# Optimization experiments

Measured on AMD Instinct MI355X. Metric: run time of the kernel, lower is better.

The kernel has to match this reference:

```python
import jax, jax.numpy as jnp
import numpy as np
import math


def _proj(x, W, b):
    # 1x1 conv: x [B,C,H,W], W [O,C], b [O]
    return jnp.einsum('bchw,oc->bohw', x, W) + b[None, :, None, None]


def _head(x, Win, bin_, Wh, bh, Wout, bout):
    # in-layer ProjConv (no skip) with ReLU
    h = jax.nn.relu(_proj(x, Win, bin_))
    # hidden ProjConv layers with skip connection (kernel_size == 1 branch)
    for i in range(Wh.shape[0]):  # static small layer count
        h = h + jax.nn.relu(_proj(h, Wh[i], bh[i]))
    # out-layer ProjConv (logits, no activation)
    return _proj(h, Wout, bout)


def _forward(x, cls_Win, cls_bin, cls_Wh, cls_bh, cls_Wout, cls_bout,
             obj_Win, obj_bin, obj_Wh, obj_bh, obj_Wout, obj_bout,
             box_Win, box_bin, box_Wh, box_bh, box_Wout, box_bout,
             pos_Win, pos_bin, pos_Wh, pos_bh, pos_Wout, pos_bout,
             ins_Win, ins_bin, ins_Wh, ins_bh, ins_Wout, ins_bout):
    cls_logits = _head(x, cls_Win, cls_bin, cls_Wh, cls_bh, cls_Wout, cls_bout)  # [B,81,H,W]
    obj_logits = _head(x, obj_Win, obj_bin, obj_Wh, obj_bh, obj_Wout, obj_bout)  # [B,2,H,W]
    box_logits = _head(x, box_Win, box_bin, box_Wh, box_bh, box_Wout, box_bout)  # [B,4,H,W]
    pos_feats = _head(x, pos_Win, pos_bin, pos_Wh, pos_bh, pos_Wout, pos_bout)   # [B,64,H,W]
    ins_feats = _head(x, ins_Win, ins_bin, ins_Wh, ins_bh, ins_Wout, ins_bout)   # [B,128,H,W]
    return jnp.concatenate([cls_logits, obj_logits, box_logits, pos_feats, ins_feats], axis=1)


def setup_inputs() -> dict:
    key = jax.random.key(0)
    ks = iter(jax.random.split(key, 64))
    F, Cin, L = 64, 64, 2
    d = {'x': jax.random.normal(next(ks), (4, Cin, 256, 256), dtype=jnp.float32)}
    outs = {'cls': 81, 'obj': 2, 'box': 4, 'pos': 64, 'ins': 128}
    prior_bias = -math.log((1.0 - 0.01) / 0.01)  # prior_prob init for cls/obj out biases
    bias0 = {'cls': prior_bias, 'obj': prior_bias, 'box': 0.0, 'pos': 0.0, 'ins': 0.0}
    for name, od in outs.items():
        d[name + '_Win'] = (jax.random.normal(next(ks), (F, Cin)) * 0.05).astype(jnp.float32)
        d[name + '_bin'] = jnp.zeros((F,), dtype=jnp.float32)
        d[name + '_Wh'] = (jax.random.normal(next(ks), (L, F, F)) * 0.05).astype(jnp.float32)
        d[name + '_bh'] = jnp.zeros((L, F), dtype=jnp.float32)
        d[name + '_Wout'] = (jax.random.normal(next(ks), (od, F)) * 0.05).astype(jnp.float32)
        d[name + '_bout'] = jnp.full((od,), bias0[name], dtype=jnp.float32)
    return d


def reference(x, cls_Win, cls_bin, cls_Wh, cls_bh, cls_Wout, cls_bout,
              obj_Win, obj_bin, obj_Wh, obj_bh, obj_Wout, obj_bout,
              box_Win, box_bin, box_Wh, box_bh, box_Wout, box_bout,
              pos_Win, pos_bin, pos_Wh, pos_bh, pos_Wout, pos_bout,
              ins_Win, ins_bin, ins_Wh, ins_bh, ins_Wout, ins_bout):
    return _forward(x, cls_Win, cls_bin, cls_Wh, cls_bh, cls_Wout, cls_bout,
                    obj_Win, obj_bin, obj_Wh, obj_bh, obj_Wout, obj_bout,
                    box_Win, box_bin, box_Wh, box_bh, box_Wout, box_bout,
                    pos_Win, pos_bin, pos_Wh, pos_bh, pos_Wout, pos_bout,
                    ins_Win, ins_bin, ins_Wh, ins_bh, ins_Wout, ins_bout)
```

## Files before the change

kernel.cpp:

```cpp
#include <hip/hip_runtime.h>

typedef unsigned short u16;
typedef unsigned int   u32;
typedef __attribute__((ext_vector_type(8)))  short bf16x8;
typedef __attribute__((ext_vector_type(4)))  float f32x4;
typedef __attribute__((ext_vector_type(16))) float f32x16;

constexpr int NPIX = 4 * 65536;

__device__ constexpr int OD_[5]   = {81, 2, 4, 64, 128};
__device__ constexpr int NFO_[5]  = {3, 1, 1, 2, 4};
__device__ constexpr int COFF_[5] = {0, 81, 83, 87, 151};
__device__ constexpr int FB_[5]   = {0, 36, 64, 92, 124};

struct PW { const float* w[20]; };
struct PB { const float* x; float* out; const u16* wf; const float* b[20]; };

__device__ __forceinline__ void split2(float v, short& hi, short& lo) {
    u32 bi = __builtin_bit_cast(u32, v);
    float lof = v - __builtin_bit_cast(float, bi & 0xffff0000u);
    hi = (short)(bi >> 16);
    lo = (short)(__builtin_bit_cast(u32, lof) >> 16);
}

__global__ __launch_bounds__(256) void prep_weights(PW wp, u16* wf) {
    int slot = blockIdx.x * 256 + threadIdx.x;
    if (slot >= 164 * 64) return;
    int frag = slot >> 6, lane = slot & 63;
    int fb = 0, seg = 0;
    for (int s = 0; s < 20; ++s) {
        int h = s >> 2, ly = s & 3;
        int cnt = (ly < 3) ? 8 : 4 * NFO_[h];
        if (frag < fb + cnt) { seg = s; break; }
        fb += cnt;
    }
    int h = seg >> 2, ly = seg & 3;
    int lf = frag - fb;
    int nf = lf >> 2, ks = lf & 3;
    int col  = nf * 32 + (lane & 31);
    int ksrc = ks * 16 + (lane >> 5) * 8;
    int rows = (ly < 3) ? 64 : OD_[h];
    const float* W = wp.w[seg];
    float wv[8];
    if (col < rows) {
        const float4* q = reinterpret_cast<const float4*>(W + col * 64 + ksrc);
        float4 a = q[0], c = q[1];
        wv[0]=a.x; wv[1]=a.y; wv[2]=a.z; wv[3]=a.w;
        wv[4]=c.x; wv[5]=c.y; wv[6]=c.z; wv[7]=c.w;
    } else {
#pragma unroll
        for (int j = 0; j < 8; ++j) wv[j] = 0.f;
    }
    bf16x8 vh, vl;
#pragma unroll
    for (int j = 0; j < 8; ++j) { short a, b; split2(wv[j], a, b); vh[j]=a; vl[j]=b; }
    u16* dst = wf + (size_t)frag * 1024 + lane * 8;
    *(bf16x8*)dst         = vh;
    *(bf16x8*)(dst + 512) = vl;
}

__device__ __forceinline__ u32 hswz(int row, int ch) {
    return (u32)((row << 8) + (ch << 2)) ^ (u32)((row & 7) << 4);
}

__device__ __forceinline__ void load_a(const char* H, int arow, int ks, int hb,
                                       bf16x8& ah, bf16x8& al) {
    u32 o0 = hswz(arow, ks * 16 + hb);
    f32x4 q0 = *(const f32x4*)(H + o0);
    f32x4 q1 = *(const f32x4*)(H + (o0 ^ 16));
    float qa[8] = {q0.x, q0.y, q0.z, q0.w, q1.x, q1.y, q1.z, q1.w};
#pragma unroll
    for (int j = 0; j < 8; ++j) { short a, b; split2(qa[j], a, b); ah[j]=a; al[j]=b; }
}

template<bool SKIP, bool FROM_LDS>
__device__ __forceinline__ void proj_layer(const bf16x8* Xh, const bf16x8* Xl,
                                           char* H, const u16* wfb,
                                           const float* bias, int l) {
    int hb = (l >> 5) * 8, arow = l & 31, hi4 = (l >> 5) * 4;
    f32x16 acc0, acc1;
#pragma unroll
    for (int i = 0; i < 16; ++i) { acc0[i] = 0.f; acc1[i] = 0.f; }
#pragma unroll
    for (int ks = 0; ks < 4; ++ks) {
        bf16x8 ah, al;
        if (FROM_LDS) load_a(H, arow, ks, hb, ah, al);
        else          { ah = Xh[ks]; al = Xl[ks]; }
        const u16* f0 = wfb + (size_t)ks * 1024;
        const u16* f1 = wfb + (size_t)(4 + ks) * 1024;
        bf16x8 b0h = *(const bf16x8*)f0, b0l = *(const bf16x8*)(f0 + 512);
        bf16x8 b1h = *(const bf16x8*)f1, b1l = *(const bf16x8*)(f1 + 512);
        acc0 = __builtin_amdgcn_mfma_f32_32x32x16_bf16(ah, b0h, acc0, 0, 0, 0);
        acc0 = __builtin_amdgcn_mfma_f32_32x32x16_bf16(ah, b0l, acc0, 0, 0, 0);
        acc0 = __builtin_amdgcn_mfma_f32_32x32x16_bf16(al, b0h, acc0, 0, 0, 0);
        acc1 = __builtin_amdgcn_mfma_f32_32x32x16_bf16(ah, b1h, acc1, 0, 0, 0);
        acc1 = __builtin_amdgcn_mfma_f32_32x32x16_bf16(ah, b1l, acc1, 0, 0, 0);
        acc1 = __builtin_amdgcn_mfma_f32_32x32x16_bf16(al, b1h, acc1, 0, 0, 0);
    }
    auto epi = [&](const f32x16& acc, int nf) {
        int ch = nf * 32 + (l & 31);
        float bv = bias[ch];
#pragma unroll
        for (int reg = 0; reg < 16; ++reg) {
            int row = (reg & 3) + 8 * (reg >> 2) + hi4;
            u32 off = hswz(row, ch);
            float v = fmaxf(acc[reg] + bv, 0.f);
            if (SKIP) v += *(const float*)(H + off);
            *(float*)(H + off) = v;
        }
    };
    epi(acc0, 0);
    epi(acc1, 1);
}

__device__ __forceinline__ void out_layer(const char* H, const u16* wfb,
                                          const float* bout, int od, int nfo,
                                          float* op_base, int l) {
    int hb = (l >> 5) * 8, arow = l & 31, hi4 = (l >> 5) * 4;
    bf16x8 Ah[4], Al[4];
#pragma unroll
    for (int ks = 0; ks < 4; ++ks) load_a(H, arow, ks, hb, Ah[ks], Al[ks]);
    for (int nf = 0; nf < nfo; ++nf) {
        f32x16 acc;
#pragma unroll
        for (int i = 0; i < 16; ++i) acc[i] = 0.f;
#pragma unroll
        for (int ks = 0; ks < 4; ++ks) {
            const u16* f = wfb + (size_t)(nf * 4 + ks) * 1024;
            bf16x8 bh = *(const bf16x8*)f, bl = *(const bf16x8*)(f + 512);
            acc = __builtin_amdgcn_mfma_f32_32x32x16_bf16(Ah[ks], bh, acc, 0, 0, 0);
            acc = __builtin_amdgcn_mfma_f32_32x32x16_bf16(Ah[ks], bl, acc, 0, 0, 0);
            acc = __builtin_amdgcn_mfma_f32_32x32x16_bf16(Al[ks], bh, acc, 0, 0, 0);
        }
        int col = nf * 32 + (l & 31);
        if (col < od) {
            float bv = bout[col];
            float* op = op_base + ((size_t)col << 16);
#pragma unroll
            for (int g = 0; g < 4; ++g) {
                int r0 = 8 * g + hi4;
                f32x4 st = {acc[4*g+0] + bv, acc[4*g+1] + bv,
                            acc[4*g+2] + bv, acc[4*g+3] + bv};
                __builtin_nontemporal_store(st, (f32x4*)(op + r0));
            }
        }
    }
}

__global__ __launch_bounds__(256, 4) void heads_main(PB p) {
    __shared__ char Hs[4][8192];
    int tid = threadIdx.x, w = tid >> 6, l = tid & 63;
    char* H = Hs[w];
    int p0 = blockIdx.x * 128 + w * 32;
    int b = p0 >> 16, hw0 = p0 & 65535;
    int hb = (l >> 5) * 8;
    const float* xb = p.x + ((size_t)(b * 64) << 16) + hw0 + (l & 31);

    bf16x8 Xh[4], Xl[4];
#pragma unroll
    for (int ks = 0; ks < 4; ++ks)
#pragma unroll
        for (int j = 0; j < 8; ++j) {
            int ch = ks * 16 + hb + j;
            float v = xb[(size_t)ch << 16];
            short a, c; split2(v, a, c);
            Xh[ks][j] = a; Xl[ks][j] = c;
        }

    const u16* wfl = p.wf + l * 8;
    for (int h = 0; h < 5; ++h) {
        const u16* wfb = wfl + (size_t)FB_[h] * 1024;
        proj_layer<false, false>(Xh, Xl, H, wfb,              p.b[4*h+0], l);
        proj_layer<true,  true >(Xh, Xl, H, wfb +  8 * 1024,  p.b[4*h+1], l);
        proj_layer<true,  true >(Xh, Xl, H, wfb + 16 * 1024,  p.b[4*h+2], l);
        float* op = p.out + ((size_t)(b * 279 + COFF_[h]) << 16) + hw0;
        out_layer(H, wfb + 24 * 1024, p.b[4*h+3], OD_[h], NFO_[h], op, l);
    }
}

extern "C" void kernel_launch(void* const* d_in, const int* in_sizes, int n_in,
                              void* d_out, int out_size, void* d_ws, size_t ws_size,
                              hipStream_t stream)
{
    auto A = [&](int i) { return (const float*)d_in[i]; };
    PW wp; PB pb;
    for (int h = 0; h < 5; ++h) {
        wp.w[4*h+0] = A(1 + 6*h + 0);
        wp.w[4*h+1] = A(1 + 6*h + 2);
        wp.w[4*h+2] = A(1 + 6*h + 2) + 4096;
        wp.w[4*h+3] = A(1 + 6*h + 4);
        pb.b[4*h+0] = A(1 + 6*h + 1);
        pb.b[4*h+1] = A(1 + 6*h + 3);
        pb.b[4*h+2] = A(1 + 6*h + 3) + 64;
        pb.b[4*h+3] = A(1 + 6*h + 5);
    }
    u16* wf = (u16*)d_ws;
    pb.x = (const float*)d_in[0];
    pb.out = (float*)d_out;
    pb.wf = wf;

    prep_weights<<<41, 256, 0, stream>>>(wp, wf);
    heads_main<<<NPIX / 128, 256, 0, stream>>>(pb);
}
```

Baseline: 609.7 us.

## Software-pipeline weight fragment loads across layers with templated per-head bodies

Restructures each head into a fully unrolled templated body that keeps an 8-deep register ring of weight fragments, prefetching the next fragment right after each MFMA triple so global weight loads overlap compute across layer boundaries. The head loop is unrolled with compile-time output fragment counts. It also replaces nontemporal output stores with normal stores and lowers the occupancy hint from 4 to 3 waves per SIMD to make room for the extra registers, which may reduce latency hiding from other waves.

```diff
diff --git a/kernel.cpp b/kernel.cpp
--- a/kernel.cpp
+++ b/kernel.cpp
@@ -10,7 +10,6 @@
 
 __device__ constexpr int OD_[5]   = {81, 2, 4, 64, 128};
 __device__ constexpr int NFO_[5]  = {3, 1, 1, 2, 4};
-__device__ constexpr int COFF_[5] = {0, 81, 83, 87, 151};
 __device__ constexpr int FB_[5]   = {0, 36, 64, 92, 124};
 
 struct PW { const float* w[20]; };
@@ -73,64 +72,90 @@
     for (int j = 0; j < 8; ++j) { short a, b; split2(qa[j], a, b); ah[j]=a; al[j]=b; }
 }
 
-template<bool SKIP, bool FROM_LDS>
-__device__ __forceinline__ void proj_layer(const bf16x8* Xh, const bf16x8* Xl,
-                                           char* H, const u16* wfb,
-                                           const float* bias, int l) {
+#define MFMA3(ACC, AH, AL, BH, BL)                                              \
+    ACC = __builtin_amdgcn_mfma_f32_32x32x16_bf16(AH, BH, ACC, 0, 0, 0);        \
+    ACC = __builtin_amdgcn_mfma_f32_32x32x16_bf16(AH, BL, ACC, 0, 0, 0);        \
+    ACC = __builtin_amdgcn_mfma_f32_32x32x16_bf16(AL, BH, ACC, 0, 0, 0);
+
+template<int NFO>
+__device__ __forceinline__ void head_body(const bf16x8* Xh, const bf16x8* Xl,
+                                          char* H, const u16* wfb,
+                                          const float* b0, const float* b1,
+                                          const float* b2, const float* bout,
+                                          int od, float* op_base, int l) {
+    constexpr int NFRAG = 24 + 4 * NFO;
     int hb = (l >> 5) * 8, arow = l & 31, hi4 = (l >> 5) * 4;
-    f32x16 acc0, acc1;
-#pragma unroll
-    for (int i = 0; i < 16; ++i) { acc0[i] = 0.f; acc1[i] = 0.f; }
-#pragma unroll
-    for (int ks = 0; ks < 4; ++ks) {
-        bf16x8 ah, al;
-        if (FROM_LDS) load_a(H, arow, ks, hb, ah, al);
-        else          { ah = Xh[ks]; al = Xl[ks]; }
-        const u16* f0 = wfb + (size_t)ks * 1024;
-        const u16* f1 = wfb + (size_t)(4 + ks) * 1024;
-        bf16x8 b0h = *(const bf16x8*)f0, b0l = *(const bf16x8*)(f0 + 512);
-        bf16x8 b1h = *(const bf16x8*)f1, b1l = *(const bf16x8*)(f1 + 512);
-        acc0 = __builtin_amdgcn_mfma_f32_32x32x16_bf16(ah, b0h, acc0, 0, 0, 0);
-        acc0 = __builtin_amdgcn_mfma_f32_32x32x16_bf16(ah, b0l, acc0, 0, 0, 0);
-        acc0 = __builtin_amdgcn_mfma_f32_32x32x16_bf16(al, b0h, acc0, 0, 0, 0);
-        acc1 = __builtin_amdgcn_mfma_f32_32x32x16_bf16(ah, b1h, acc1, 0, 0, 0);
-        acc1 = __builtin_amdgcn_mfma_f32_32x32x16_bf16(ah, b1l, acc1, 0, 0, 0);
-        acc1 = __builtin_amdgcn_mfma_f32_32x32x16_bf16(al, b1h, acc1, 0, 0, 0);
-    }
-    auto epi = [&](const f32x16& acc, int nf) {
-        int ch = nf * 32 + (l & 31);
-        float bv = bias[ch];
-#pragma unroll
-        for (int reg = 0; reg < 16; ++reg) {
-            int row = (reg & 3) + 8 * (reg >> 2) + hi4;
-            u32 off = hswz(row, ch);
-            float v = fmaxf(acc[reg] + bv, 0.f);
-            if (SKIP) v += *(const float*)(H + off);
-            *(float*)(H + off) = v;
-        }
-    };
-    epi(acc0, 0);
-    epi(acc1, 1);
-}
-
-__device__ __forceinline__ void out_layer(const char* H, const u16* wfb,
-                                          const float* bout, int od, int nfo,
-                                          float* op_base, int l) {
-    int hb = (l >> 5) * 8, arow = l & 31, hi4 = (l >> 5) * 4;
+
+    bf16x8 Ph[8], Pl[8];
+#pragma unroll
+    for (int f = 0; f < 8; ++f) {
+        const u16* fp = wfb + (size_t)f * 1024;
+        Ph[f] = *(const bf16x8*)fp;
+        Pl[f] = *(const bf16x8*)(fp + 512);
+    }
+
+#pragma unroll
+    for (int ly = 0; ly < 3; ++ly) {
+        bf16x8 Ah[4], Al[4];
+#pragma unroll
+        for (int ks = 0; ks < 4; ++ks) {
+            if (ly == 0) { Ah[ks] = Xh[ks]; Al[ks] = Xl[ks]; }
+            else         load_a(H, arow, ks, hb, Ah[ks], Al[ks]);
+        }
+        const float* bias = (ly == 0) ? b0 : ((ly == 1) ? b1 : b2);
+        f32x16 acc0, acc1;
+#pragma unroll
+        for (int i = 0; i < 16; ++i) { acc0[i] = 0.f; acc1[i] = 0.f; }
+#pragma unroll
+        for (int nf = 0; nf < 2; ++nf)
+#pragma unroll
+            for (int ks = 0; ks < 4; ++ks) {
+                int fi = ly * 8 + nf * 4 + ks;
+                int c  = fi & 7;
+                if (nf == 0) { MFMA3(acc0, Ah[ks], Al[ks], Ph[c], Pl[c]); }
+                else         { MFMA3(acc1, Ah[ks], Al[ks], Ph[c], Pl[c]); }
+                int nx = fi + 8;
+                if (nx < NFRAG) {
+                    const u16* fp = wfb + (size_t)nx * 1024;
+                    Ph[c] = *(const bf16x8*)fp;
+                    Pl[c] = *(const bf16x8*)(fp + 512);
+                }
+            }
+#pragma unroll
+        for (int nf = 0; nf < 2; ++nf) {
+            int ch = nf * 32 + (l & 31);
+            float bv = bias[ch];
+#pragma unroll
+            for (int reg = 0; reg < 16; ++reg) {
+                int row = (reg & 3) + 8 * (reg >> 2) + hi4;
+                u32 off = hswz(row, ch);
+                float a = (nf == 0) ? acc0[reg] : acc1[reg];
+                float v = fmaxf(a + bv, 0.f);
+                if (ly > 0) v += *(const float*)(H + off);
+                *(float*)(H + off) = v;
+            }
+        }
+    }
+
     bf16x8 Ah[4], Al[4];
 #pragma unroll
     for (int ks = 0; ks < 4; ++ks) load_a(H, arow, ks, hb, Ah[ks], Al[ks]);
-    for (int nf = 0; nf < nfo; ++nf) {
+#pragma unroll
+    for (int nf = 0; nf < NFO; ++nf) {
         f32x16 acc;
 #pragma unroll
         for (int i = 0; i < 16; ++i) acc[i] = 0.f;
 #pragma unroll
         for (int ks = 0; ks < 4; ++ks) {
-            const u16* f = wfb + (size_t)(nf * 4 + ks) * 1024;
-            bf16x8 bh = *(const bf16x8*)f, bl = *(const bf16x8*)(f + 512);
-            acc = __builtin_amdgcn_mfma_f32_32x32x16_bf16(Ah[ks], bh, acc, 0, 0, 0);
-            acc = __builtin_amdgcn_mfma_f32_32x32x16_bf16(Ah[ks], bl, acc, 0, 0, 0);
-            acc = __builtin_amdgcn_mfma_f32_32x32x16_bf16(Al[ks], bh, acc, 0, 0, 0);
+            int fi = 24 + nf * 4 + ks;
+            int c  = fi & 7;
+            MFMA3(acc, Ah[ks], Al[ks], Ph[c], Pl[c]);
+            int nx = fi + 8;
+            if (nx < NFRAG) {
+                const u16* fp = wfb + (size_t)nx * 1024;
+                Ph[c] = *(const bf16x8*)fp;
+                Pl[c] = *(const bf16x8*)(fp + 512);
+            }
         }
         int col = nf * 32 + (l & 31);
         if (col < od) {
@@ -141,13 +166,13 @@
                 int r0 = 8 * g + hi4;
                 f32x4 st = {acc[4*g+0] + bv, acc[4*g+1] + bv,
                             acc[4*g+2] + bv, acc[4*g+3] + bv};
-                __builtin_nontemporal_store(st, (f32x4*)(op + r0));
-            }
-        }
-    }
-}
-
-__global__ __launch_bounds__(256, 4) void heads_main(PB p) {
+                *(f32x4*)(op + r0) = st;
+            }
+        }
+    }
+}
+
+__global__ __launch_bounds__(256, 3) void heads_main(PB p) {
     __shared__ char Hs[4][8192];
     int tid = threadIdx.x, w = tid >> 6, l = tid & 63;
     char* H = Hs[w];
@@ -168,14 +193,12 @@
         }
 
     const u16* wfl = p.wf + l * 8;
-    for (int h = 0; h < 5; ++h) {
-        const u16* wfb = wfl + (size_t)FB_[h] * 1024;
-        proj_layer<false, false>(Xh, Xl, H, wfb,              p.b[4*h+0], l);
-        proj_layer<true,  true >(Xh, Xl, H, wfb +  8 * 1024,  p.b[4*h+1], l);
-        proj_layer<true,  true >(Xh, Xl, H, wfb + 16 * 1024,  p.b[4*h+2], l);
-        float* op = p.out + ((size_t)(b * 279 + COFF_[h]) << 16) + hw0;
-        out_layer(H, wfb + 24 * 1024, p.b[4*h+3], OD_[h], NFO_[h], op, l);
-    }
+    size_t ob = ((size_t)b * 279) << 16;
+    head_body<3>(Xh, Xl, H, wfl + (size_t)FB_[0] * 1024, p.b[0],  p.b[1],  p.b[2],  p.b[3],   81, p.out + ob + (((size_t)  0) << 16) + hw0, l);
+    head_body<1>(Xh, Xl, H, wfl + (size_t)FB_[1] * 1024, p.b[4],  p.b[5],  p.b[6],  p.b[7],    2, p.out + ob + (((size_t) 81) << 16) + hw0, l);
+    head_body<1>(Xh, Xl, H, wfl + (size_t)FB_[2] * 1024, p.b[8],  p.b[9],  p.b[10], p.b[11],   4, p.out + ob + (((size_t) 83) << 16) + hw0, l);
+    head_body<2>(Xh, Xl, H, wfl + (size_t)FB_[3] * 1024, p.b[12], p.b[13], p.b[14], p.b[15],  64, p.out + ob + (((size_t) 87) << 16) + hw0, l);
+    head_body<4>(Xh, Xl, H, wfl + (size_t)FB_[4] * 1024, p.b[16], p.b[17], p.b[18], p.b[19], 128, p.out + ob + (((size_t)151) << 16) + hw0, l);
 }
 
 extern "C" void kernel_launch(void* const* d_in, const int* in_sizes, int n_in,
```

Measured after the change: 531.1 us. -12.9%, faster.
